# Kernel optimization log

Hardware: AMD Instinct MI355X
Metric: run time of the kernel (lower is better)

Reference implementation:

```python
import jax, jax.numpy as jnp
import numpy as np

K = 3          # kernel size
PAD = 1        # padding
# deformable conv v2: offset conv (2*K*K ch), modulator conv (K*K ch, 2*sigmoid), main 3x3 conv, ReLU


def _conv2d(x, w, b):
    y = jax.lax.conv_general_dilated(x, w, (1, 1), ((PAD, PAD), (PAD, PAD)),
                                     dimension_numbers=('NCHW', 'OIHW', 'NCHW'))
    return y + b[None, :, None, None]


def _bilinear_gather(x, py, px):
    # x: [B,C,H,W]; py/px: [B,K2,H,W] float sample coords; zero outside image.
    B, C, H, W = x.shape
    y0 = jnp.floor(py)
    x0 = jnp.floor(px)
    wy1 = py - y0
    wx1 = px - x0
    wy0 = 1.0 - wy1
    wx0 = 1.0 - wx1
    xf = x.reshape(B, C, H * W)

    def gather(yi, xi):
        valid = (yi >= 0) & (yi <= H - 1) & (xi >= 0) & (xi <= W - 1)
        yc = jnp.clip(yi, 0, H - 1).astype(jnp.int32)
        xc = jnp.clip(xi, 0, W - 1).astype(jnp.int32)
        idx = (yc * W + xc).reshape(B, -1)                      # [B, K2*H*W]
        v = jax.vmap(lambda xb, ib: xb[:, ib])(xf, idx)         # [B, C, K2*H*W]
        v = v.reshape(B, C, *yi.shape[1:])                      # [B, C, K2, H, W]
        return v * valid[:, None].astype(x.dtype)

    return (gather(y0, x0) * (wy0 * wx0)[:, None]
            + gather(y0, x0 + 1) * (wy0 * wx1)[:, None]
            + gather(y0 + 1, x0) * (wy1 * wx0)[:, None]
            + gather(y0 + 1, x0 + 1) * (wy1 * wx1)[:, None])


def _deform_conv(data, w, b, w_off, b_off, w_mod, b_mod):
    B, Cin, H, W = data.shape
    off = _conv2d(data, w_off, b_off)                           # [B, 2*K2, H, W]
    mask = 2.0 * jax.nn.sigmoid(_conv2d(data, w_mod, b_mod))    # [B, K2, H, W]
    off = off.reshape(B, K * K, 2, H, W)                        # (dy, dx) per tap
    dy, dx = off[:, :, 0], off[:, :, 1]
    ki, kj = jnp.meshgrid(jnp.arange(K), jnp.arange(K), indexing='ij')
    ki = ki.reshape(-1).astype(data.dtype)
    kj = kj.reshape(-1).astype(data.dtype)
    hs = jnp.arange(H, dtype=data.dtype)
    ws = jnp.arange(W, dtype=data.dtype)
    py = hs[None, None, :, None] - PAD + ki[None, :, None, None] + dy
    px = ws[None, None, None, :] - PAD + kj[None, :, None, None] + dx
    sampled = _bilinear_gather(data, py, px)                    # [B, Cin, K2, H, W]
    sampled = sampled * mask[:, None]
    out = jnp.einsum('bckhw,ock->bohw', sampled, w.reshape(w.shape[0], Cin, K * K))
    return out + b[None, :, None, None]


def setup_inputs() -> dict:
    key = jax.random.key(0)
    ks = jax.random.split(key, 7)
    B, Cin, Cout, H, W = 8, 64, 64, 128, 128
    fan = Cin * K * K
    return {
        'data': jax.random.normal(ks[0], (B, Cin, H, W), jnp.float32),
        'w': jax.random.normal(ks[1], (Cout, Cin, K, K), jnp.float32) / np.sqrt(fan),
        'b': jax.random.normal(ks[2], (Cout,), jnp.float32) * 0.01,
        'w_off': jax.random.normal(ks[3], (2 * K * K, Cin, K, K), jnp.float32) * (0.1 / np.sqrt(fan)),
        'b_off': jnp.zeros((2 * K * K,), jnp.float32),
        'w_mod': jax.random.normal(ks[4], (K * K, Cin, K, K), jnp.float32) * (0.1 / np.sqrt(fan)),
        'b_mod': jnp.zeros((K * K,), jnp.float32),
    }


def reference(data, w, b, w_off, b_off, w_mod, b_mod):
    return jax.nn.relu(_deform_conv(data, w, b, w_off, b_off, w_mod, b_mod))
```

## Files before the change

kernel.cpp:

```cpp
#include <hip/hip_runtime.h>
#include <hip/hip_fp16.h>
#include <cstdint>


typedef _Float16 half8 __attribute__((ext_vector_type(8)));
typedef __attribute__((ext_vector_type(4))) float floatx4;

__device__ __forceinline__ unsigned int pack2h(float lo, float hi) {
    __half2 h = __floats2half2_rn(lo, hi);
    union { __half2 h; unsigned int u; } cv; cv.h = h;
    return cv.u;
}
__device__ __forceinline__ unsigned int blend2h(unsigned int a, unsigned int b,
                                                unsigned int c, unsigned int d,
                                                const __half2* w) {
    union { unsigned int u; __half2 h; } A, B, C, D, O;
    A.u = a; B.u = b; C.u = c; D.u = d;
    __half2 s = __hmul2(A.h, w[0]);
    s = __hfma2(B.h, w[1], s);
    s = __hfma2(C.h, w[2], s);
    s = __hfma2(D.h, w[3], s);
    O.h = s;
    return O.u;
}

#define OFF_DATAT 0u
#define OFF_WM    16777216u
#define OFF_W27   16850944u
#define OFF_B27   16887808u

__global__ __launch_bounds__(256) void prep_k(const float* __restrict__ x,
                                              unsigned short* __restrict__ xt,
                                              const float* __restrict__ w,
                                              const float* __restrict__ w_off,
                                              const float* __restrict__ w_mod,
                                              const float* __restrict__ b_off,
                                              const float* __restrict__ b_mod,
                                              unsigned short* __restrict__ wpackM,
                                              unsigned short* __restrict__ wpack27,
                                              float* __restrict__ bias27) {
    __shared__ float tile[64][65];
    int blk = blockIdx.x;
    if (blk < 2048) {
        int b    = blk >> 8;
        int pos0 = (blk & 255) << 6;
        int lane = threadIdx.x & 63;
        int g    = threadIdx.x >> 6;
        for (int c = g; c < 64; c += 4)
            tile[c][lane] = x[(((b << 6) + c) << 14) + pos0 + lane];
        __syncthreads();
        int c2 = lane & 31;
        for (int i = g; i < 32; i += 4) {
            int pr = (i << 1) + (lane >> 5);
            unsigned int d = pack2h(tile[c2 << 1][pr], tile[(c2 << 1) + 1][pr]);
            *(unsigned int*)&xt[((size_t)((b << 14) + pos0 + pr) << 6) + (c2 << 1)] = d;
        }
        return;
    }
    int t = (blk - 2048) * 256 + threadIdx.x;
    if (t < 64 * 576) {
        int o = t / 576, kk = t % 576;
        int k = kk >> 6, c = kk & 63;
        wpackM[t] = __half_as_ushort(__float2half_rn(w[(o * 64 + c) * 9 + k]));
        return;
    }
    t -= 64 * 576;
    if (t < 32 * 576) {
        int o = t / 576, kk = t % 576;
        int k = kk >> 6, c = kk & 63;
        float v = 0.f;
        if (o < 18)      v = w_off[(o * 64 + c) * 9 + k];
        else if (o < 27) v = w_mod[((o - 18) * 64 + c) * 9 + k];
        wpack27[t] = __half_as_ushort(__float2half_rn(v));
        if (kk == 0) bias27[o] = (o < 18) ? b_off[o] : (o < 27 ? b_mod[o - 18] : 0.f);
    }
}

__global__ __launch_bounds__(256, 3) void deform_main_k(const unsigned short* __restrict__ xt,
                                                        const unsigned short* __restrict__ wpackM,
                                                        const unsigned short* __restrict__ wpack27,
                                                        const float* __restrict__ bias27,
                                                        const float* __restrict__ bias,
                                                        float* __restrict__ out) {
    __shared__ __align__(16) char ldsbuf[35680];
    ushort4*        pOff   = (ushort4*)(ldsbuf);
    uint4*          pW     = (uint4*)(ldsbuf + 4608);
    unsigned short (*samp)[64][72]   = (unsigned short (*)[64][72])(ldsbuf + 13824);
    unsigned short (*tile27)[66][72] = (unsigned short (*)[66][72])(ldsbuf);
    float          (*pp)[28]         = (float (*)[28])(ldsbuf + 28512);

    int blk  = blockIdx.x;
    int b    = blk >> 8;
    int pos0 = (blk & 255) << 6;
    int tid  = threadIdx.x;
    int lane = tid & 63, wv = tid >> 6;
    int r = lane & 15, q = lane >> 4;
    int pg = lane >> 3;
    int j8 = lane & 7;

    const unsigned short* xb = xt + ((size_t)b << 20);
    const char* xbb = (const char*)xb;

    {
        int row = pos0 >> 7;
        int c0  = pos0 & 127;
        for (int e = tid; e < 1584; e += 256) {
            int rr  = e / 528;
            int rem = e - rr * 528;
            int cc  = rem >> 3;
            int j   = rem & 7;
            int sy  = row - 1 + rr;
            int sx  = c0 - 1 + cc;
            uint4 v = {0u, 0u, 0u, 0u};
            if (sy >= 0 && sy < 128 && sx >= 0 && sx < 128)
                v = *(const uint4*)&xb[(size_t)(((sy << 7) + sx) << 6) + (j << 3)];
            *(uint4*)&tile27[rr][cc][j << 3] = v;
        }
        __syncthreads();

        floatx4 acc27[2] = {};
        #pragma unroll
        for (int k = 0; k < 9; ++k) {
            int ki = k / 3, kj = k % 3;
            #pragma unroll
            for (int chh = 0; chh < 2; ++chh) {
                half8 a0 = *(const half8*)&wpack27[(r)      * 576 + (k << 6) + (chh << 5) + (q << 3)];
                half8 a1 = *(const half8*)&wpack27[(16 + r) * 576 + (k << 6) + (chh << 5) + (q << 3)];
                half8 bf = *(const half8*)&tile27[ki][(wv << 4) + r + kj][(chh << 5) + (q << 3)];
                acc27[0] = __builtin_amdgcn_mfma_f32_16x16x32_f16(a0, bf, acc27[0], 0, 0, 0);
                acc27[1] = __builtin_amdgcn_mfma_f32_16x16x32_f16(a1, bf, acc27[1], 0, 0, 0);
            }
        }
        #pragma unroll
        for (int s = 0; s < 2; ++s) {
            #pragma unroll
            for (int reg = 0; reg < 4; ++reg) {
                int oc = (s << 4) + (q << 2) + reg;
                if (oc < 27) {
                    float v = acc27[s][reg] + bias27[oc];
                    if (oc >= 18) v = 2.f / (1.f + __expf(-v));
                    pp[(wv << 4) + r][oc] = v;
                }
            }
        }
        __syncthreads();
    }

    for (int e = tid; e < 576; e += 256) {
        int k = e >> 6, p = e & 63;
        int pos = pos0 + p;
        float dy = pp[p][(k << 1)];
        float dx = pp[p][(k << 1) + 1];
        float m  = pp[p][18 + k];
        float py = (float)(pos >> 7) + (float)(k / 3 - 1) + dy;
        float px = (float)(pos & 127) + (float)(k % 3 - 1) + dx;
        float y0f = floorf(py), x0f = floorf(px);
        int y0 = (int)y0f, x0 = (int)x0f;
        float wy1 = py - y0f, wx1 = px - x0f;
        float wy0 = 1.f - wy1, wx0 = 1.f - wx1;
        bool vy0 = (y0 >= 0) && (y0 < 128);
        bool vy1 = (y0 >= -1) && (y0 < 127);
        bool vx0 = (x0 >= 0) && (x0 < 128);
        bool vx1 = (x0 >= -1) && (x0 < 127);
        float w00 = (vy0 && vx0) ? m * wy0 * wx0 : 0.f;
        float w01 = (vy0 && vx1) ? m * wy0 * wx1 : 0.f;
        float w10 = (vy1 && vx0) ? m * wy1 * wx0 : 0.f;
        float w11 = (vy1 && vx1) ? m * wy1 * wx1 : 0.f;
        int y0c = min(max(y0, 0), 127), y1c = min(max(y0 + 1, 0), 127);
        int x0c = min(max(x0, 0), 127), x1c = min(max(x0 + 1, 0), 127);
        ushort4 io;
        io.x = (unsigned short)((y0c << 7) + x0c);
        io.y = (unsigned short)((y0c << 7) + x1c);
        io.z = (unsigned short)((y1c << 7) + x0c);
        io.w = (unsigned short)((y1c << 7) + x1c);
        pOff[e] = io;
        union { uint4 u; __half2 h[4]; } pw;
        pw.h[0] = __float2half2_rn(w00);
        pw.h[1] = __float2half2_rn(w01);
        pw.h[2] = __float2half2_rn(w10);
        pw.h[3] = __float2half2_rn(w11);
        pW[e] = pw.u;
    }
    __syncthreads();

    floatx4 acc[4] = {};
    const char* xp = xbb + (j8 << 4);
    const unsigned short* wrow = wpackM + ((wv << 4) + r) * 576 + (q << 3);

    uint4   c00[2][2], c01[2][2], c10[2][2], c11[2][2];
    uint4   cwS[2][2];
    ushort4 nio[2];
    uint4   ncw[2];
    half8   afC[2], afN[2];

    auto readParams = [&](int k) {
        #pragma unroll
        for (int i = 0; i < 2; ++i) {
            int e  = (k << 6) + (wv << 4) + (i << 3) + pg;
            nio[i] = pOff[e];
            ncw[i] = pW[e];
        }
    };
    auto issueInto = [&](int s) {
        #pragma unroll
        for (int i = 0; i < 2; ++i) {
            cwS[s][i] = ncw[i];
            c00[s][i] = *(const uint4*)(xp + ((int)nio[i].x << 7));
            c01[s][i] = *(const uint4*)(xp + ((int)nio[i].y << 7));
            c10[s][i] = *(const uint4*)(xp + ((int)nio[i].z << 7));
            c11[s][i] = *(const uint4*)(xp + ((int)nio[i].w << 7));
        }
    };
    auto blendStore = [&](int s, int buf) {
        #pragma unroll
        for (int i = 0; i < 2; ++i) {
            int p = (wv << 4) + (i << 3) + pg;
            union { uint4 u; __half2 h[4]; } W; W.u = cwS[s][i];
            uint4 o4;
            o4.x = blend2h(c00[s][i].x, c01[s][i].x, c10[s][i].x, c11[s][i].x, W.h);
            o4.y = blend2h(c00[s][i].y, c01[s][i].y, c10[s][i].y, c11[s][i].y, W.h);
            o4.z = blend2h(c00[s][i].z, c01[s][i].z, c10[s][i].z, c11[s][i].z, W.h);
            o4.w = blend2h(c00[s][i].w, c01[s][i].w, c10[s][i].w, c11[s][i].w, W.h);
            *(uint4*)&samp[buf][p][j8 << 3] = o4;
        }
    };

    auto ldsBarrier = [&]() {
        asm volatile("s_waitcnt lgkmcnt(0)\n\ts_barrier" ::: "memory");
    };

    readParams(0); issueInto(0);
    readParams(1); issueInto(1);
    afC[0] = *(const half8*)&wrow[0];
    afC[1] = *(const half8*)&wrow[32];
    blendStore(0, 0);
    readParams(2);

    #pragma unroll
    for (int k = 0; k < 9; ++k) {
        if (k <= 6) issueInto(k & 1);
        if (k < 8) {
            afN[0] = *(const half8*)&wrow[((k + 1) << 6)];
            afN[1] = *(const half8*)&wrow[((k + 1) << 6) + 32];
        }
        ldsBarrier();
        #pragma unroll
        for (int ch = 0; ch < 2; ++ch) {
            #pragma unroll
            for (int nt = 0; nt < 4; ++nt) {
                half8 bfrag = *(const half8*)&samp[k & 1][(nt << 4) + r][(ch << 5) + (q << 3)];
                acc[nt] = __builtin_amdgcn_mfma_f32_16x16x32_f16(afC[ch], bfrag, acc[nt], 0, 0, 0);
            }
        }
        if (k < 8) {
            blendStore((k + 1) & 1, (k + 1) & 1);
            if (k <= 5) readParams(k + 3);
            afC[0] = afN[0];
            afC[1] = afN[1];
        }
    }

    #pragma unroll
    for (int nt = 0; nt < 4; ++nt) {
        #pragma unroll
        for (int reg = 0; reg < 4; ++reg) {
            int oc  = (wv << 4) + (q << 2) + reg;
            int pos = pos0 + (nt << 4) + r;
            float v = acc[nt][reg] + bias[oc];
            out[(size_t)(((b << 6) + oc) << 14) + pos] = fmaxf(v, 0.f);
        }
    }
}

extern "C" void kernel_launch(void* const* d_in, const int* in_sizes, int n_in,
                              void* d_out, int out_size, void* d_ws, size_t ws_size,
                              hipStream_t stream) {
    const float* data  = (const float*)d_in[0];
    const float* w     = (const float*)d_in[1];
    const float* bias  = (const float*)d_in[2];
    const float* w_off = (const float*)d_in[3];
    const float* b_off = (const float*)d_in[4];
    const float* w_mod = (const float*)d_in[5];
    const float* b_mod = (const float*)d_in[6];
    float* out = (float*)d_out;

    char* ws = (char*)d_ws;
    unsigned short* dataT   = (unsigned short*)(ws + OFF_DATAT);
    unsigned short* wpackM  = (unsigned short*)(ws + OFF_WM);
    unsigned short* wpack27 = (unsigned short*)(ws + OFF_W27);
    float*          bias27  = (float*)(ws + OFF_B27);

    prep_k<<<2264, 256, 0, stream>>>(data, dataT, w, w_off, w_mod,
                                     b_off, b_mod, wpackM, wpack27, bias27);
    deform_main_k<<<2048, 256, 0, stream>>>(dataT, wpackM, wpack27, bias27, bias, out);
}
```

Measured before the change: 169.5 us.

## Stage 5x68 input window in LDS and gather bilinear taps from it

Measured after the change: 185.5 us. +9.5%, slower.

```diff
diff --git a/kernel.cpp b/kernel.cpp
--- a/kernel.cpp
+++ b/kernel.cpp
@@ -28,6 +28,11 @@
 #define OFF_WM    16777216u
 #define OFF_W27   16850944u
 #define OFF_B27   16887808u
+
+#define L_SAMP 43520
+#define L_POFF 61952
+#define L_PW   66560
+#define L_TOTAL 75776
 
 __global__ __launch_bounds__(256) void prep_k(const float* __restrict__ x,
                                               unsigned short* __restrict__ xt,
@@ -76,22 +81,25 @@
     }
 }
 
-__global__ __launch_bounds__(256, 3) void deform_main_k(const unsigned short* __restrict__ xt,
+__global__ __launch_bounds__(256, 2) void deform_main_k(const unsigned short* __restrict__ xt,
                                                         const unsigned short* __restrict__ wpackM,
                                                         const unsigned short* __restrict__ wpack27,
                                                         const float* __restrict__ bias27,
                                                         const float* __restrict__ bias,
                                                         float* __restrict__ out) {
-    __shared__ __align__(16) char ldsbuf[35680];
-    ushort4*        pOff   = (ushort4*)(ldsbuf);
-    uint4*          pW     = (uint4*)(ldsbuf + 4608);
-    unsigned short (*samp)[64][72]   = (unsigned short (*)[64][72])(ldsbuf + 13824);
-    unsigned short (*tile27)[66][72] = (unsigned short (*)[66][72])(ldsbuf);
-    float          (*pp)[28]         = (float (*)[28])(ldsbuf + 28512);
+    extern __shared__ __align__(16) char lds[];
+    char*           winB = lds;
+    unsigned short (*samp)[64][72] = (unsigned short (*)[64][72])(lds + L_SAMP);
+    float          (*pp)[28]       = (float (*)[28])(lds + L_SAMP);
+    ushort4*        pOff = (ushort4*)(lds + L_POFF);
+    uint4*          pW   = (uint4*)(lds + L_PW);
 
     int blk  = blockIdx.x;
     int b    = blk >> 8;
     int pos0 = (blk & 255) << 6;
+    int row  = pos0 >> 7;
+    int c0   = pos0 & 127;
+    int rbase = row - 2, cbase = c0 - 2;
     int tid  = threadIdx.x;
     int lane = tid & 63, wv = tid >> 6;
     int r = lane & 15, q = lane >> 4;
@@ -101,23 +109,22 @@
     const unsigned short* xb = xt + ((size_t)b << 20);
     const char* xbb = (const char*)xb;
 
+    for (int e = tid; e < 2720; e += 256) {
+        int rr  = e / 544;
+        int rem = e - rr * 544;
+        int cc  = rem >> 3;
+        int jd  = rem & 7;
+        int sy  = rbase + rr, sx = cbase + cc;
+        uint4 v = {0u, 0u, 0u, 0u};
+        if (sy >= 0 && sy < 128 && sx >= 0 && sx < 128) {
+            int js = jd ^ (cc & 7);
+            v = *(const uint4*)&xb[(size_t)(((sy << 7) + sx) << 6) + (js << 3)];
+        }
+        *(uint4*)(winB + (((rr * 68) + cc) << 7) + (jd << 4)) = v;
+    }
+    __syncthreads();
+
     {
-        int row = pos0 >> 7;
-        int c0  = pos0 & 127;
-        for (int e = tid; e < 1584; e += 256) {
-            int rr  = e / 528;
-            int rem = e - rr * 528;
-            int cc  = rem >> 3;
-            int j   = rem & 7;
-            int sy  = row - 1 + rr;
-            int sx  = c0 - 1 + cc;
-            uint4 v = {0u, 0u, 0u, 0u};
-            if (sy >= 0 && sy < 128 && sx >= 0 && sx < 128)
-                v = *(const uint4*)&xb[(size_t)(((sy << 7) + sx) << 6) + (j << 3)];
-            *(uint4*)&tile27[rr][cc][j << 3] = v;
-        }
-        __syncthreads();
-
         floatx4 acc27[2] = {};
         #pragma unroll
         for (int k = 0; k < 9; ++k) {
@@ -126,7 +133,10 @@
             for (int chh = 0; chh < 2; ++chh) {
                 half8 a0 = *(const half8*)&wpack27[(r)      * 576 + (k << 6) + (chh << 5) + (q << 3)];
                 half8 a1 = *(const half8*)&wpack27[(16 + r) * 576 + (k << 6) + (chh << 5) + (q << 3)];
-                half8 bf = *(const half8*)&tile27[ki][(wv << 4) + r + kj][(chh << 5) + (q << 3)];
+                int cc = (wv << 4) + r + kj + 1;
+                int rr = ki + 1;
+                int chunk = ((chh << 2) + q) ^ (cc & 7);
+                half8 bf = *(const half8*)(winB + (((rr * 68) + cc) << 7) + (chunk << 4));
                 acc27[0] = __builtin_amdgcn_mfma_f32_16x16x32_f16(a0, bf, acc27[0], 0, 0, 0);
                 acc27[1] = __builtin_amdgcn_mfma_f32_16x16x32_f16(a1, bf, acc27[1], 0, 0, 0);
             }
@@ -143,8 +153,8 @@
                 }
             }
         }
-        __syncthreads();
-    }
+    }
+    __syncthreads();
 
     for (int e = tid; e < 576; e += 256) {
         int k = e >> 6, p = e & 63;
@@ -168,11 +178,17 @@
         float w11 = (vy1 && vx1) ? m * wy1 * wx1 : 0.f;
         int y0c = min(max(y0, 0), 127), y1c = min(max(y0 + 1, 0), 127);
         int x0c = min(max(x0, 0), 127), x1c = min(max(x0 + 1, 0), 127);
+        auto enc = [&](int y, int x) -> unsigned short {
+            int iy = y - rbase, ix = x - cbase;
+            if ((unsigned)iy < 5u && (unsigned)ix < 68u)
+                return (unsigned short)((iy * 68 + ix) | ((ix & 7) << 12));
+            return (unsigned short)(0x8000u | (unsigned)((y << 7) + x));
+        };
         ushort4 io;
-        io.x = (unsigned short)((y0c << 7) + x0c);
-        io.y = (unsigned short)((y0c << 7) + x1c);
-        io.z = (unsigned short)((y1c << 7) + x0c);
-        io.w = (unsigned short)((y1c << 7) + x1c);
+        io.x = enc(y0c, x0c);
+        io.y = enc(y0c, x1c);
+        io.z = enc(y1c, x0c);
+        io.w = enc(y1c, x1c);
         pOff[e] = io;
         union { uint4 u; __half2 h[4]; } pw;
         pw.h[0] = __float2half2_rn(w00);
@@ -187,8 +203,8 @@
     const char* xp = xbb + (j8 << 4);
     const unsigned short* wrow = wpackM + ((wv << 4) + r) * 576 + (q << 3);
 
-    uint4   c00[2][2], c01[2][2], c10[2][2], c11[2][2];
-    uint4   cwS[2][2];
+    uint4   c00[2], c01[2], c10[2], c11[2];
+    uint4   cw[2];
     ushort4 nio[2];
     uint4   ncw[2];
     half8   afC[2], afN[2];
@@ -201,60 +217,88 @@
             ncw[i] = pW[e];
         }
     };
-    auto issueInto = [&](int s) {
-        #pragma unroll
-        for (int i = 0; i < 2; ++i) {
-            cwS[s][i] = ncw[i];
-            c00[s][i] = *(const uint4*)(xp + ((int)nio[i].x << 7));
-            c01[s][i] = *(const uint4*)(xp + ((int)nio[i].y << 7));
-            c10[s][i] = *(const uint4*)(xp + ((int)nio[i].z << 7));
-            c11[s][i] = *(const uint4*)(xp + ((int)nio[i].w << 7));
-        }
-    };
-    auto blendStore = [&](int s, int buf) {
+    auto ldwin = [&](unsigned int u) -> uint4 {
+        int idx = (int)(u & 0xFFFu);
+        int s   = (int)((u >> 12) & 7u);
+        return *(const uint4*)(winB + (idx << 7) + ((j8 ^ s) << 4));
+    };
+    auto ldany = [&](unsigned int u) -> uint4 {
+        int pos;
+        if (u & 0x8000u) pos = (int)(u & 0x7FFFu);
+        else {
+            int idx = (int)(u & 0xFFFu);
+            int iy = idx / 68, ix = idx - iy * 68;
+            pos = ((rbase + iy) << 7) + (cbase + ix);
+        }
+        return *(const uint4*)(xp + ((size_t)pos << 7));
+    };
+    auto gather = [&]() {
+        unsigned int mm = (unsigned)nio[0].x | nio[0].y | nio[0].z | nio[0].w
+                        | nio[1].x | nio[1].y | nio[1].z | nio[1].w;
+        if (__all((mm & 0x8000u) == 0)) {
+            #pragma unroll
+            for (int i = 0; i < 2; ++i) {
+                cw[i]  = ncw[i];
+                c00[i] = ldwin(nio[i].x);
+                c01[i] = ldwin(nio[i].y);
+                c10[i] = ldwin(nio[i].z);
+                c11[i] = ldwin(nio[i].w);
+            }
+        } else {
+            #pragma unroll
+            for (int i = 0; i < 2; ++i) {
+                cw[i]  = ncw[i];
+                c00[i] = ldany(nio[i].x);
+                c01[i] = ldany(nio[i].y);
+                c10[i] = ldany(nio[i].z);
+                c11[i] = ldany(nio[i].w);
+            }
+        }
+    };
+    auto blendStore = [&](int buf) {
         #pragma unroll
         for (int i = 0; i < 2; ++i) {
             int p = (wv << 4) + (i << 3) + pg;
-            union { uint4 u; __half2 h[4]; } W; W.u = cwS[s][i];
+            union { uint4 u; __half2 h[4]; } W; W.u = cw[i];
             uint4 o4;
-            o4.x = blend2h(c00[s][i].x, c01[s][i].x, c10[s][i].x, c11[s][i].x, W.h);
-            o4.y = blend2h(c00[s][i].y, c01[s][i].y, c10[s][i].y, c11[s][i].y, W.h);
-            o4.z = blend2h(c00[s][i].z, c01[s][i].z, c10[s][i].z, c11[s][i].z, W.h);
-            o4.w = blend2h(c00[s][i].w, c01[s][i].w, c10[s][i].w, c11[s][i].w, W.h);
+            o4.x = blend2h(c00[i].x, c01[i].x, c10[i].x, c11[i].x, W.h);
+            o4.y = blend2h(c00[i].y, c01[i].y, c10[i].y, c11[i].y, W.h);
+            o4.z = blend2h(c00[i].z, c01[i].z, c10[i].z, c11[i].z, W.h);
+            o4.w = blend2h(c00[i].w, c01[i].w, c10[i].w, c11[i].w, W.h);
             *(uint4*)&samp[buf][p][j8 << 3] = o4;
         }
     };
-
     auto ldsBarrier = [&]() {
         asm volatile("s_waitcnt lgkmcnt(0)\n\ts_barrier" ::: "memory");
     };
 
-    readParams(0); issueInto(0);
-    readParams(1); issueInto(1);
+    readParams(0); gather(); blendStore(0);
+    readParams(1);
     afC[0] = *(const half8*)&wrow[0];
     afC[1] = *(const half8*)&wrow[32];
-    blendStore(0, 0);
-    readParams(2);
 
     #pragma unroll
     for (int k = 0; k < 9; ++k) {
-        if (k <= 6) issueInto(k & 1);
         if (k < 8) {
             afN[0] = *(const half8*)&wrow[((k + 1) << 6)];
             afN[1] = *(const half8*)&wrow[((k + 1) << 6) + 32];
         }
         ldsBarrier();
-        #pragma unroll
-        for (int ch = 0; ch < 2; ++ch) {
-            #pragma unroll
-            for (int nt = 0; nt < 4; ++nt) {
-                half8 bfrag = *(const half8*)&samp[k & 1][(nt << 4) + r][(ch << 5) + (q << 3)];
-                acc[nt] = __builtin_amdgcn_mfma_f32_16x16x32_f16(afC[ch], bfrag, acc[nt], 0, 0, 0);
-            }
-        }
+        half8 bf[2][4];
+        #pragma unroll
+        for (int ch = 0; ch < 2; ++ch)
+            #pragma unroll
+            for (int nt = 0; nt < 4; ++nt)
+                bf[ch][nt] = *(const half8*)&samp[k & 1][(nt << 4) + r][(ch << 5) + (q << 3)];
+        if (k < 8) gather();
+        #pragma unroll
+        for (int ch = 0; ch < 2; ++ch)
+            #pragma unroll
+            for (int nt = 0; nt < 4; ++nt)
+                acc[nt] = __builtin_amdgcn_mfma_f32_16x16x32_f16(afC[ch], bf[ch][nt], acc[nt], 0, 0, 0);
         if (k < 8) {
-            blendStore((k + 1) & 1, (k + 1) & 1);
-            if (k <= 5) readParams(k + 3);
+            blendStore((k + 1) & 1);
+            if (k <= 6) readParams(k + 2);
             afC[0] = afN[0];
             afC[1] = afN[1];
         }
@@ -290,7 +334,15 @@
     unsigned short* wpack27 = (unsigned short*)(ws + OFF_W27);
     float*          bias27  = (float*)(ws + OFF_B27);
 
+    static bool s_attr = false;
+    if (!s_attr) {
+        hipFuncSetAttribute((const void*)deform_main_k,
+                            hipFuncAttributeMaxDynamicSharedMemorySize, L_TOTAL);
+        s_attr = true;
+    }
+
     prep_k<<<2264, 256, 0, stream>>>(data, dataT, w, w_off, w_mod,
                                      b_off, b_mod, wpackM, wpack27, bias27);
-    deform_main_k<<<2048, 256, 0, stream>>>(dataT, wpackM, wpack27, bias27, bias, out);
-}
+    deform_main_k<<<2048, 256, L_TOTAL, stream>>>(dataT, wpackM, wpack27,
+                                                  bias27, bias, out);
+}
```
